# Kernel optimization log

Measured on AMD Instinct MI355X. Metric: run time of the kernel, lower is better.

The kernel has to match this reference:

```python
import jax, jax.numpy as jnp
import numpy as np
from jax import lax

C, HID, NCLS, CDIM = 16, 128, 32, 64

def _dwconv(x, k):
    # x: [B,C,H,W], k: [C,1,3,3] depthwise (groups=C), SAME padding
    return lax.conv_general_dilated(
        x, k, window_strides=(1, 1), padding='SAME',
        dimension_numbers=('NCHW', 'OIHW', 'NCHW'), feature_group_count=x.shape[1])

def setup_inputs() -> dict:
    key = jax.random.key(0)
    ks = jax.random.split(key, 10)
    B, H, W = 4, 256, 256
    Fin = 3 * C
    inp = {
        'x': jax.random.normal(ks[0], (B, C, H, W), jnp.float32),
        'cond': jax.random.randint(ks[1], (B,), 0, NCLS, jnp.int32),
        'embed': jax.random.normal(ks[2], (NCLS, CDIM), jnp.float32) * 0.1,
        # Linear weights stored as [in, out] (transposed torch layout)
        'film_w': jax.random.normal(ks[3], (CDIM, 2 * HID), jnp.float32) * (1.0 / np.sqrt(CDIM)),
        'film_b': jnp.zeros((2 * HID,), jnp.float32),
        'fc1_w': jax.random.normal(ks[4], (Fin, HID), jnp.float32) * (1.0 / np.sqrt(Fin)),
        'fc1_b': jnp.zeros((HID,), jnp.float32),
        'fc2_w': jax.random.normal(ks[5], (HID, HID), jnp.float32) * (1.0 / np.sqrt(HID)),
        'fc2_b': jnp.zeros((HID,), jnp.float32),
        # fc3 is zero-init in the module; use small random values so output != input
        'fc3_w': jax.random.normal(ks[6], (HID, C), jnp.float32) * 0.01,
        'fc3_b': jnp.zeros((C,), jnp.float32),
        'n_steps': 4,
    }
    return inp

def reference(x, cond, embed, film_w, film_b, fc1_w, fc1_b, fc2_w, fc2_b, fc3_w, fc3_b, n_steps):
    sx = jnp.array([[-1., 0., 1.], [-2., 0., 2.], [-1., 0., 1.]], jnp.float32)
    kx = jnp.tile(sx[None, None], (C, 1, 1, 1))   # [C,1,3,3]
    ky = jnp.tile(sx.T[None, None], (C, 1, 1, 1))

    # FiLM params are step-invariant: compute once
    film = embed[cond] @ film_w + film_b          # [B, 2*HID]
    gamma, beta = jnp.split(film, 2, axis=1)      # [B, HID] each
    gamma = gamma[:, None, None, :]               # [B,1,1,HID]
    beta = beta[:, None, None, :]

    def step(xs, _):
        gx = _dwconv(xs, kx)
        gy = _dwconv(xs, ky)
        feats = jnp.concatenate([xs, gx, gy], axis=1).transpose(0, 2, 3, 1)  # [B,H,W,3C]
        h = jax.nn.relu(feats @ fc1_w + fc1_b)
        h = gamma * h + beta
        h = jax.nn.relu(h @ fc2_w + fc2_b)
        dx = (h @ fc3_w + fc3_b).transpose(0, 3, 1, 2)                        # [B,C,H,W]
        dx = jnp.clip(dx, -10.0, 10.0)
        return xs + dx * 0.1, None

    out, _ = lax.scan(step, x, None, length=n_steps)
    return out
```

## Files before the change

### kernel.cpp

```cpp
#include <hip/hip_runtime.h>

typedef __bf16 bf16x8 __attribute__((ext_vector_type(8)));
typedef float f32x4 __attribute__((ext_vector_type(4)));
typedef float f32x16 __attribute__((ext_vector_type(16)));
typedef unsigned int u32x4 __attribute__((ext_vector_type(4)));

#define FILM_WS 0
#define W1_WS   4096
#define W2B_WS  20480
#define W3_WS   151552
#define B2_WS   159744
#define XBUF_WS 163840

#define W1_OFF  0
#define W2_OFF  16384
#define W3_OFF  49152
#define XL_OFF  57344
#define LDS_TOTAL 109568

static __device__ __forceinline__ unsigned short f2bf(float f) {
  unsigned int u = __builtin_bit_cast(unsigned int, f);
  u += 0x7fffu + ((u >> 16) & 1u);
  return (unsigned short)(u >> 16);
}

static __device__ __forceinline__ unsigned cvtpk(float lo, float hi) {
  unsigned r;
  asm("v_cvt_pk_bf16_f32 %0, %1, %2" : "=v"(r) : "v"(lo), "v"(hi));
  return r;
}

static __device__ __forceinline__ void plswap(unsigned &a, unsigned &b) {
  auto r = __builtin_amdgcn_permlane32_swap((int)a, (int)b, false, false);
  a = (unsigned)r[0];
  b = (unsigned)r[1];
}

static __device__ __forceinline__ f32x16 MF(bf16x8 a, bf16x8 b, f32x16 c) {
  return __builtin_amdgcn_mfma_f32_32x32x16_bf16(a, b, c, 0, 0, 0);
}

template <int OFF>
static __device__ __forceinline__ u32x4 cvt2(f32x16 a) {
  unsigned A0 = cvtpk(fmaxf(a[OFF + 0], 0.f), fmaxf(a[OFF + 1], 0.f));
  unsigned A1 = cvtpk(fmaxf(a[OFF + 2], 0.f), fmaxf(a[OFF + 3], 0.f));
  unsigned B0 = cvtpk(fmaxf(a[OFF + 4], 0.f), fmaxf(a[OFF + 5], 0.f));
  unsigned B1 = cvtpk(fmaxf(a[OFF + 6], 0.f), fmaxf(a[OFF + 7], 0.f));
  plswap(A0, B0); plswap(A1, B1);
  return (u32x4){A0, A1, B0, B1};
}

#define ZERO16 (f32x16){0.f,0.f,0.f,0.f,0.f,0.f,0.f,0.f,0.f,0.f,0.f,0.f,0.f,0.f,0.f,0.f}
#define LDW(off) __builtin_bit_cast(bf16x8, *(const u32x4*)(sm + (off)))
#define U2B(v)   __builtin_bit_cast(bf16x8, v)

__global__ __launch_bounds__(256) void prep_film(
    const int* __restrict__ cond, const float* __restrict__ embed,
    const float* __restrict__ film_w, const float* __restrict__ film_b,
    char* __restrict__ ws) {
  int id = blockIdx.x * 256 + threadIdx.x;
  int b = id >> 8, j = id & 255;
  const float* e = embed + cond[b] * 64;
  float s = film_b[j];
  #pragma unroll 8
  for (int k = 0; k < 64; ++k) s += e[k] * film_w[k * 256 + j];
  ((float*)(ws + FILM_WS))[b * 256 + j] = s;
}

__global__ __launch_bounds__(256) void prep_w(
    const float* __restrict__ fc1w, const float* __restrict__ fc1b,
    const float* __restrict__ fc2w, const float* __restrict__ fc2b,
    const float* __restrict__ fc3w, char* __restrict__ ws) {
  int id = blockIdx.x * 256 + threadIdx.x;
  const float* film = (const float*)(ws + FILM_WS);
  if (id < 8192) {
    int n = id >> 6, k = id & 63;
    float v = (k < 48) ? fc1w[k * 128 + n] : (k == 48 ? fc1b[n] : 0.f);
    *(unsigned short*)(ws + W1_WS + ((n * 128 + 2 * k) ^ ((n & 7) << 4))) = f2bf(v);
  } else if (id < 8192 + 65536) {
    int t = id - 8192; int bb = t >> 14; t &= 16383;
    int n = t >> 7, k = t & 127;
    float v = film[bb * 256 + k] * fc2w[k * 128 + n];
    *(unsigned short*)(ws + W2B_WS + bb * 32768 + ((n * 256 + 2 * k) ^ ((n & 15) << 4))) = f2bf(v);
  } else if (id < 8192 + 65536 + 4096) {
    int t = id - 73728; int n = t >> 7, k = t & 127;
    float v = (n < 16) ? fc3w[k * 16 + n] : 0.f;
    *(unsigned short*)(ws + W3_WS + ((n * 256 + 2 * k) ^ ((n & 15) << 4))) = f2bf(v);
  } else if (id < 8192 + 65536 + 4096 + 512) {
    int t = id - 77824; int bb = t >> 7, n = t & 127;
    float s = fc2b[n];
    for (int k = 0; k < 128; ++k)
      s += film[bb * 256 + 128 + k] * fc2w[k * 128 + n];
    ((float*)(ws + B2_WS))[bb * 128 + n] = s;
  }
}

#define G1NT(nt, ZA, ZB) do {                                               \
    const int n_ = (nt) * 32 + l31;                                         \
    const int rb_ = n_ * 128, sw_ = (n_ & 7) << 4;                          \
    bf16x8 wA_ = LDW(W1_OFF + ((rb_ +  0 + 16 * h5) ^ sw_));                \
    bf16x8 wB_ = LDW(W1_OFF + ((rb_ + 32 + 16 * h5) ^ sw_));                \
    bf16x8 wC_ = LDW(W1_OFF + ((rb_ + 64 + 16 * h5) ^ sw_));                \
    bf16x8 wD_ = LDW(W1_OFF + ((rb_ + 96 + 16 * h5) ^ sw_));                \
    f32x16 a_ = ZERO16;                                                     \
    a_ = MF(wA_, fx,  a_);                                                  \
    a_ = MF(wB_, fgx, a_);                                                  \
    a_ = MF(wC_, fgy, a_);                                                  \
    a_ = MF(wD_, fone, a_);                                                 \
    ZA = cvt2<0>(a_); ZB = cvt2<8>(a_);                                     \
  } while (0)

#define K2(kk) do {                                                         \
    bf16x8 wf_ = LDW(W2_OFF + ((rb2_ + 32 * (kk) + 16 * h5) ^ sw2_));       \
    a_ = MF(wf_, U2B(z##kk), a_);                                           \
  } while (0)

#define G23NT(nt) do {                                                      \
    const int n_ = (nt) * 32 + l31;                                         \
    const int rb2_ = n_ * 256, sw2_ = (n_ & 15) << 4;                       \
    f32x16 a_ = ZERO16;                                                     \
    K2(0); K2(1); K2(2); K2(3); K2(4); K2(5); K2(6); K2(7);                 \
    bf16x8 wb_ = U2B(((u32x4){wb2##nt, 0u, 0u, 0u}));                       \
    a_ = MF(wb_, fone, a_);                                                 \
    u32x4 hA_ = cvt2<0>(a_), hB_ = cvt2<8>(a_);                             \
    bf16x8 w3a_ = LDW(W3_OFF + ((rb3 + 32 * (2 * (nt))     + 16 * h5) ^ sw3)); \
    bf16x8 w3b_ = LDW(W3_OFF + ((rb3 + 32 * (2 * (nt) + 1) + 16 * h5) ^ sw3)); \
    cacc = MF(w3a_, U2B(hA_), cacc);                                        \
    cacc = MF(w3b_, U2B(hB_), cacc);                                        \
  } while (0)

__global__ __launch_bounds__(512)
__attribute__((amdgpu_waves_per_eu(2, 2)))
void step_kernel(
    const float* __restrict__ xin, float* __restrict__ xout,
    const char* __restrict__ ws, const float* __restrict__ fc3b) {
  __shared__ __attribute__((aligned(16))) char sm[LDS_TOTAL];
  float* smf = (float*)(sm + XL_OFF);
  const int tid = threadIdx.x;
  const int bid = blockIdx.x;
  const int b = bid >> 6, idx = bid & 63;
  const int h0 = idx * 4;

  for (int i = tid; i < 3584; i += 512) {
    const char* src; int dst;
    if (i < 1024)      { src = ws + W1_WS + i * 16;                       dst = W1_OFF + i * 16; }
    else if (i < 3072) { src = ws + W2B_WS + b * 32768 + (i - 1024) * 16; dst = W2_OFF + (i - 1024) * 16; }
    else               { src = ws + W3_WS + (i - 3072) * 16;              dst = W3_OFF + (i - 3072) * 16; }
    *(u32x4*)(sm + dst) = *(const u32x4*)src;
  }

  const int lane = tid & 63, wv = tid >> 6;
  const int l31 = lane & 31, h5 = lane >> 5;
  const int band = wv * 64;
  const int p0 = band + l31,      p1 = band + 32 + l31;
  const int pr0 = p0 >> 7, pc0 = p0 & 127;
  const int pr1 = p1 >> 7, pc1 = p1 & 127;
  const int cbase = h5 * 8;
  const unsigned bONE = (h5 == 0) ? 0x3F80u : 0u;
  const bf16x8 fone = U2B(((u32x4){bONE, 0u, 0u, 0u}));
  const int rb3 = l31 * 256, sw3 = (l31 & 15) << 4;

  const float* b2p = (const float*)(ws + B2_WS) + b * 128 + l31;
  const unsigned wb20 = (h5 == 0) ? cvtpk(b2p[0],  0.f) : 0u;
  const unsigned wb21 = (h5 == 0) ? cvtpk(b2p[32], 0.f) : 0u;
  const unsigned wb22 = (h5 == 0) ? cvtpk(b2p[64], 0.f) : 0u;
  const unsigned wb23 = (h5 == 0) ? cvtpk(b2p[96], 0.f) : 0u;
  const float b3v = (l31 < 16) ? fc3b[l31] : 0.f;
  const unsigned wb3 = (h5 == 0) ? cvtpk(b3v, 0.f) : 0u;

  const int iseg = tid >> 5, iq = tid & 31;
  const int eseg = tid >> 1, ee = tid & 1;

  #pragma unroll
  for (int j = 0; j < 2; ++j) {
    const int w0 = j << 7;
    __syncthreads();
    {
      f32x4 t0 = {0,0,0,0}, t1 = {0,0,0,0}, t2 = {0,0,0,0},
            t3 = {0,0,0,0}, t4 = {0,0,0,0}, t5 = {0,0,0,0};
      float te = 0.f;
      #define HLOAD(T, K) do {                                              \
          int seg_ = iseg + 16 * (K);                                       \
          int c_ = seg_ / 6, dh_ = seg_ - 6 * c_;                           \
          int g_ = h0 - 1 + dh_;                                            \
          if ((unsigned)g_ < 256u)                                          \
            T = *(const f32x4*)(xin + (((b * 16 + c_) * 256 + g_) << 8) + w0 + 4 * iq); \
        } while (0)
      HLOAD(t0, 0); HLOAD(t1, 1); HLOAD(t2, 2);
      HLOAD(t3, 3); HLOAD(t4, 4); HLOAD(t5, 5);
      #undef HLOAD
      if (tid < 192) {
        int c_ = eseg / 6, dh_ = eseg - 6 * c_;
        int g_ = h0 - 1 + dh_;
        int w_ = w0 - 1 + ee * 129;
        if ((unsigned)g_ < 256u && (unsigned)w_ < 256u)
          te = xin[(((b * 16 + c_) * 256 + g_) << 8) + w_];
      }
      *(f32x4*)(smf + (iseg +  0) * 136 + 4 + 4 * iq) = t0;
      *(f32x4*)(smf + (iseg + 16) * 136 + 4 + 4 * iq) = t1;
      *(f32x4*)(smf + (iseg + 32) * 136 + 4 + 4 * iq) = t2;
      *(f32x4*)(smf + (iseg + 48) * 136 + 4 + 4 * iq) = t3;
      *(f32x4*)(smf + (iseg + 64) * 136 + 4 + 4 * iq) = t4;
      *(f32x4*)(smf + (iseg + 80) * 136 + 4 + 4 * iq) = t5;
      if (tid < 192)
        smf[eseg * 136 + 3 + ee * 129] = te;
    }
    __syncthreads();

    auto do_group = [&](int pr, int pc) {
      bf16x8 fx, fgx, fgy;
      #pragma unroll
      for (int jc = 0; jc < 8; ++jc) {
        const float* s0 = smf + ((cbase + jc) * 6 + pr) * 136 + 3 + pc;
        float a00 = s0[0],   a01 = s0[1],   a02 = s0[2];
        float a10 = s0[136], a11 = s0[137], a12 = s0[138];
        float a20 = s0[272], a21 = s0[273], a22 = s0[274];
        fx[jc]  = (__bf16)a11;
        fgx[jc] = (__bf16)((a02 - a00) + 2.f * (a12 - a10) + (a22 - a20));
        fgy[jc] = (__bf16)((a20 - a00) + 2.f * (a21 - a01) + (a22 - a02));
      }

      u32x4 z0, z1, z2, z3, z4, z5, z6, z7;
      G1NT(0, z0, z1);
      G1NT(1, z2, z3);
      G1NT(2, z4, z5);
      G1NT(3, z6, z7);

      f32x16 cacc = ZERO16;
      G23NT(0); G23NT(1); G23NT(2); G23NT(3);
      {
        bf16x8 wb_ = U2B(((u32x4){wb3, 0u, 0u, 0u}));
        cacc = MF(wb_, fone, cacc);
      }

      #pragma unroll
      for (int r = 0; r < 8; ++r) {
        const int c = 4 * h5 + (r & 3) + 8 * (r >> 2);
        float dx = fminf(fmaxf(cacc[r], -10.f), 10.f);
        float xo = smf[(c * 6 + pr + 1) * 136 + 4 + pc];
        xout[(((b * 16 + c) * 256 + h0 + pr) << 8) + w0 + pc] = xo + 0.1f * dx;
      }
    };
    do_group(pr0, pc0);
    do_group(pr1, pc1);
  }
}

extern "C" void kernel_launch(void* const* d_in, const int* in_sizes, int n_in,
                              void* d_out, int out_size, void* d_ws, size_t ws_size,
                              hipStream_t stream) {
  const float* x      = (const float*)d_in[0];
  const int*   cond   = (const int*)d_in[1];
  const float* embed  = (const float*)d_in[2];
  const float* film_w = (const float*)d_in[3];
  const float* film_b = (const float*)d_in[4];
  const float* fc1w   = (const float*)d_in[5];
  const float* fc1b   = (const float*)d_in[6];
  const float* fc2w   = (const float*)d_in[7];
  const float* fc2b   = (const float*)d_in[8];
  const float* fc3w   = (const float*)d_in[9];
  const float* fc3b   = (const float*)d_in[10];

  char*  ws   = (char*)d_ws;
  float* xbuf = (float*)(ws + XBUF_WS);
  float* out  = (float*)d_out;

  prep_film<<<4, 256, 0, stream>>>(cond, embed, film_w, film_b, ws);
  prep_w<<<306, 256, 0, stream>>>(fc1w, fc1b, fc2w, fc2b, fc3w, ws);

  dim3 grid(256), blk(512);
  step_kernel<<<grid, blk, 0, stream>>>(x,    xbuf, ws, fc3b);
  step_kernel<<<grid, blk, 0, stream>>>(xbuf, out,  ws, fc3b);
  step_kernel<<<grid, blk, 0, stream>>>(out,  xbuf, ws, fc3b);
  step_kernel<<<grid, blk, 0, stream>>>(xbuf, out,  ws, fc3b);
}
```

Measured before the change: 117.5 us.

## Split tiles into smaller 2-row chunks and prefetch next halo into registers

The per-block work is restructured from two 4-row tiles, each processed as two pixel groups per thread, into four 2-row tiles with one pixel group per thread. The global loads for the next tile's halo are issued into registers before the current tile's MFMA work, so load latency overlaps compute. The smaller halo tile cuts the LDS footprint. In exchange, each block does more barriers and reloads more overlapping halo rows, and the prefetch registers raise register pressure. A small unroll pragma is also added to the bias precompute loop.

```diff
diff --git a/kernel.cpp b/kernel.cpp
--- a/kernel.cpp
+++ b/kernel.cpp
@@ -16,7 +16,7 @@
 #define W2_OFF  16384
 #define W3_OFF  49152
 #define XL_OFF  57344
-#define LDS_TOTAL 109568
+#define LDS_TOTAL 92160
 
 static __device__ __forceinline__ unsigned short f2bf(float f) {
   unsigned int u = __builtin_bit_cast(unsigned int, f);
@@ -89,6 +89,7 @@
   } else if (id < 8192 + 65536 + 4096 + 512) {
     int t = id - 77824; int bb = t >> 7, n = t & 127;
     float s = fc2b[n];
+    #pragma unroll 8
     for (int k = 0; k < 128; ++k)
       s += film[bb * 256 + 128 + k] * fc2w[k * 128 + n];
     ((float*)(ws + B2_WS))[bb * 128 + n] = s;
@@ -139,7 +140,6 @@
   const int tid = threadIdx.x;
   const int bid = blockIdx.x;
   const int b = bid >> 6, idx = bid & 63;
-  const int h0 = idx * 4;
 
   for (int i = tid; i < 3584; i += 512) {
     const char* src; int dst;
@@ -151,10 +151,8 @@
 
   const int lane = tid & 63, wv = tid >> 6;
   const int l31 = lane & 31, h5 = lane >> 5;
-  const int band = wv * 64;
-  const int p0 = band + l31,      p1 = band + 32 + l31;
-  const int pr0 = p0 >> 7, pc0 = p0 & 127;
-  const int pr1 = p1 >> 7, pc1 = p1 & 127;
+  const int p = wv * 32 + l31;
+  const int pr = p >> 7, pc = p & 127;
   const int cbase = h5 * 8;
   const unsigned bONE = (h5 == 0) ? 0x3F80u : 0u;
   const bf16x8 fone = U2B(((u32x4){bONE, 0u, 0u, 0u}));
@@ -171,78 +169,80 @@
   const int iseg = tid >> 5, iq = tid & 31;
   const int eseg = tid >> 1, ee = tid & 1;
 
+  f32x4 pre0, pre1, pre2, pre3;
+  float peg;
+  auto PREFETCH = [&](int jn) {
+    const int h0n = idx * 4 + (jn >> 1) * 2;
+    const int w0n = (jn & 1) << 7;
+    #define HLOAD(T, K) do {                                                \
+        int seg_ = iseg + 16 * (K);                                         \
+        int c_ = seg_ >> 2, dh_ = seg_ & 3;                                 \
+        int g_ = h0n - 1 + dh_;                                             \
+        T = (f32x4){0.f, 0.f, 0.f, 0.f};                                    \
+        if ((unsigned)g_ < 256u)                                            \
+          T = *(const f32x4*)(xin + (((b * 16 + c_) * 256 + g_) << 8) + w0n + 4 * iq); \
+      } while (0)
+    HLOAD(pre0, 0); HLOAD(pre1, 1); HLOAD(pre2, 2); HLOAD(pre3, 3);
+    #undef HLOAD
+    peg = 0.f;
+    if (tid < 128) {
+      int c_ = eseg >> 2, dh_ = eseg & 3;
+      int g_ = h0n - 1 + dh_;
+      int w_ = w0n - 1 + ee * 129;
+      if ((unsigned)g_ < 256u && (unsigned)w_ < 256u)
+        peg = xin[(((b * 16 + c_) * 256 + g_) << 8) + w_];
+    }
+  };
+
+  PREFETCH(0);
+
   #pragma unroll
-  for (int j = 0; j < 2; ++j) {
-    const int w0 = j << 7;
+  for (int j = 0; j < 4; ++j) {
+    const int h0 = idx * 4 + (j >> 1) * 2;
+    const int w0 = (j & 1) << 7;
     __syncthreads();
+    *(f32x4*)(smf + (iseg +  0) * 136 + 4 + 4 * iq) = pre0;
+    *(f32x4*)(smf + (iseg + 16) * 136 + 4 + 4 * iq) = pre1;
+    *(f32x4*)(smf + (iseg + 32) * 136 + 4 + 4 * iq) = pre2;
+    *(f32x4*)(smf + (iseg + 48) * 136 + 4 + 4 * iq) = pre3;
+    if (tid < 128)
+      smf[eseg * 136 + 3 + ee * 129] = peg;
+    __syncthreads();
+
+    if (j < 3) PREFETCH(j + 1);
+
+    bf16x8 fx, fgx, fgy;
+    #pragma unroll
+    for (int jc = 0; jc < 8; ++jc) {
+      const float* s0 = smf + ((cbase + jc) * 4 + pr) * 136 + 3 + pc;
+      float a00 = s0[0],   a01 = s0[1],   a02 = s0[2];
+      float a10 = s0[136], a11 = s0[137], a12 = s0[138];
+      float a20 = s0[272], a21 = s0[273], a22 = s0[274];
+      fx[jc]  = (__bf16)a11;
+      fgx[jc] = (__bf16)((a02 - a00) + 2.f * (a12 - a10) + (a22 - a20));
+      fgy[jc] = (__bf16)((a20 - a00) + 2.f * (a21 - a01) + (a22 - a02));
+    }
+
+    u32x4 z0, z1, z2, z3, z4, z5, z6, z7;
+    G1NT(0, z0, z1);
+    G1NT(1, z2, z3);
+    G1NT(2, z4, z5);
+    G1NT(3, z6, z7);
+
+    f32x16 cacc = ZERO16;
+    G23NT(0); G23NT(1); G23NT(2); G23NT(3);
     {
-      f32x4 t0 = {0,0,0,0}, t1 = {0,0,0,0}, t2 = {0,0,0,0},
-            t3 = {0,0,0,0}, t4 = {0,0,0,0}, t5 = {0,0,0,0};
-      float te = 0.f;
-      #define HLOAD(T, K) do {                                              \
-          int seg_ = iseg + 16 * (K);                                       \
-          int c_ = seg_ / 6, dh_ = seg_ - 6 * c_;                           \
-          int g_ = h0 - 1 + dh_;                                            \
-          if ((unsigned)g_ < 256u)                                          \
-            T = *(const f32x4*)(xin + (((b * 16 + c_) * 256 + g_) << 8) + w0 + 4 * iq); \
-        } while (0)
-      HLOAD(t0, 0); HLOAD(t1, 1); HLOAD(t2, 2);
-      HLOAD(t3, 3); HLOAD(t4, 4); HLOAD(t5, 5);
-      #undef HLOAD
-      if (tid < 192) {
-        int c_ = eseg / 6, dh_ = eseg - 6 * c_;
-        int g_ = h0 - 1 + dh_;
-        int w_ = w0 - 1 + ee * 129;
-        if ((unsigned)g_ < 256u && (unsigned)w_ < 256u)
-          te = xin[(((b * 16 + c_) * 256 + g_) << 8) + w_];
-      }
-      *(f32x4*)(smf + (iseg +  0) * 136 + 4 + 4 * iq) = t0;
-      *(f32x4*)(smf + (iseg + 16) * 136 + 4 + 4 * iq) = t1;
-      *(f32x4*)(smf + (iseg + 32) * 136 + 4 + 4 * iq) = t2;
-      *(f32x4*)(smf + (iseg + 48) * 136 + 4 + 4 * iq) = t3;
-      *(f32x4*)(smf + (iseg + 64) * 136 + 4 + 4 * iq) = t4;
-      *(f32x4*)(smf + (iseg + 80) * 136 + 4 + 4 * iq) = t5;
-      if (tid < 192)
-        smf[eseg * 136 + 3 + ee * 129] = te;
-    }
-    __syncthreads();
-
-    auto do_group = [&](int pr, int pc) {
-      bf16x8 fx, fgx, fgy;
-      #pragma unroll
-      for (int jc = 0; jc < 8; ++jc) {
-        const float* s0 = smf + ((cbase + jc) * 6 + pr) * 136 + 3 + pc;
-        float a00 = s0[0],   a01 = s0[1],   a02 = s0[2];
-        float a10 = s0[136], a11 = s0[137], a12 = s0[138];
-        float a20 = s0[272], a21 = s0[273], a22 = s0[274];
-        fx[jc]  = (__bf16)a11;
-        fgx[jc] = (__bf16)((a02 - a00) + 2.f * (a12 - a10) + (a22 - a20));
-        fgy[jc] = (__bf16)((a20 - a00) + 2.f * (a21 - a01) + (a22 - a02));
-      }
-
-      u32x4 z0, z1, z2, z3, z4, z5, z6, z7;
-      G1NT(0, z0, z1);
-      G1NT(1, z2, z3);
-      G1NT(2, z4, z5);
-      G1NT(3, z6, z7);
-
-      f32x16 cacc = ZERO16;
-      G23NT(0); G23NT(1); G23NT(2); G23NT(3);
-      {
-        bf16x8 wb_ = U2B(((u32x4){wb3, 0u, 0u, 0u}));
-        cacc = MF(wb_, fone, cacc);
-      }
-
-      #pragma unroll
-      for (int r = 0; r < 8; ++r) {
-        const int c = 4 * h5 + (r & 3) + 8 * (r >> 2);
-        float dx = fminf(fmaxf(cacc[r], -10.f), 10.f);
-        float xo = smf[(c * 6 + pr + 1) * 136 + 4 + pc];
-        xout[(((b * 16 + c) * 256 + h0 + pr) << 8) + w0 + pc] = xo + 0.1f * dx;
-      }
-    };
-    do_group(pr0, pc0);
-    do_group(pr1, pc1);
+      bf16x8 wb_ = U2B(((u32x4){wb3, 0u, 0u, 0u}));
+      cacc = MF(wb_, fone, cacc);
+    }
+
+    #pragma unroll
+    for (int r = 0; r < 8; ++r) {
+      const int c = 4 * h5 + (r & 3) + 8 * (r >> 2);
+      float dx = fminf(fmaxf(cacc[r], -10.f), 10.f);
+      float xo = smf[(c * 4 + pr + 1) * 136 + 4 + pc];
+      xout[(((b * 16 + c) * 256 + h0 + pr) << 8) + w0 + pc] = xo + 0.1f * dx;
+    }
   }
 }
 
```

After: 113.5 us. 3.4% less time.
